# Kernel optimization log

Hardware: AMD Instinct MI355X
Metric: run time of the kernel (lower is better)

The kernel has to match this reference:

```python
import jax, jax.numpy as jnp
import numpy as np

C_S = 128
C_T = 128
C_OUT = 128


def _proj(x, W, b):
    # 1x1x1 Conv3d == per-voxel linear over channel dim. x: [B, Cin, T, H, W]
    return jnp.einsum('oc,bcthw->bothw', W, x) + b[None, :, None, None, None]


def setup_inputs() -> dict:
    key = jax.random.key(0)
    ks = jax.random.split(key, 12)
    B, T, H, W = 4, 4, 32, 32
    spatial_features = jax.random.normal(ks[0], (B, T, C_S, H, W), dtype=jnp.float32)
    temporal_features = jax.random.normal(ks[1], (B, C_T, T, H, W), dtype=jnp.float32)
    def w(k, o, i):
        return jax.random.normal(k, (o, i), dtype=jnp.float32) * (i ** -0.5)
    return {
        'spatial_features': spatial_features,
        'temporal_features': temporal_features,
        'Wq': w(ks[2], C_OUT, C_S), 'bq': jnp.zeros((C_OUT,), jnp.float32),
        'Wk': w(ks[3], C_OUT, C_T), 'bk': jnp.zeros((C_OUT,), jnp.float32),
        'Wv': w(ks[4], C_OUT, C_T), 'bv': jnp.zeros((C_OUT,), jnp.float32),
        'Wo': w(ks[5], C_OUT, C_OUT), 'bo': jnp.zeros((C_OUT,), jnp.float32),
    }


def reference(spatial_features, temporal_features, Wq, bq, Wk, bk, Wv, bv, Wo, bo):
    B, T, C_s, H, W = spatial_features.shape
    N = T * H * W
    scale = C_OUT ** -0.5
    # permute(0,2,1,3,4): [B, T, C_s, H, W] -> [B, C_s, T, H, W]
    x_s = jnp.transpose(spatial_features, (0, 2, 1, 3, 4))
    q = _proj(x_s, Wq, bq)                 # [B, C_out, T, H, W]
    k = _proj(temporal_features, Wk, bk)   # [B, C_out, T, H, W]
    v = _proj(temporal_features, Wv, bv)   # [B, C_out, T, H, W]
    Q = q.reshape(B, C_OUT, N).transpose(0, 2, 1)  # [B, N, C]
    K = k.reshape(B, C_OUT, N)                     # [B, C, N]
    V = v.reshape(B, C_OUT, N).transpose(0, 2, 1)  # [B, N, C]
    attn = jax.nn.softmax(jnp.einsum('bnc,bcm->bnm', Q, K) * scale, axis=2)  # [B, N, N]
    out = jnp.einsum('bnm,bmc->bnc', attn, V)      # [B, N, C]
    out = out.transpose(0, 2, 1).reshape(B, C_OUT, T, H, W)
    return _proj(out, Wo, bo)
```

## Files before the change

kernel.cpp:

```cpp
#include <hip/hip_runtime.h>
#include <cstddef>

#define NDIM 4096
#define SCALE_L2E 0.12751741843533886f
#define BIAS_L2E  11.541560327111707f

typedef _Float16 h8 __attribute__((ext_vector_type(8)));
typedef _Float16 h4 __attribute__((ext_vector_type(4)));
typedef _Float16 h2 __attribute__((ext_vector_type(2)));
typedef float    f4 __attribute__((ext_vector_type(4)));

__device__ __forceinline__ void gld_lds16(const void* g, void* l) {
    __builtin_amdgcn_global_load_lds(
        (const __attribute__((address_space(1))) void*)g,
        (__attribute__((address_space(3))) void*)l, 16, 0, 0);
}

__device__ __forceinline__ h8 cvt_w_frag(const float* wp) {
    const float4 u0 = *(const float4*)wp;
    const float4 u1 = *(const float4*)(wp + 4);
    h8 f;
    f[0]=(_Float16)u0.x; f[1]=(_Float16)u0.y; f[2]=(_Float16)u0.z; f[3]=(_Float16)u0.w;
    f[4]=(_Float16)u1.x; f[5]=(_Float16)u1.y; f[6]=(_Float16)u1.z; f[7]=(_Float16)u1.w;
    return f;
}

__global__ __launch_bounds__(256) void prep_w_kernel(
    const float* __restrict__ Wq, const float* __restrict__ Wk,
    const float* __restrict__ Wv, const float* __restrict__ Wo,
    _Float16* __restrict__ Whf)
{
    const int gid = blockIdx.x * 256 + threadIdx.x;
    const int mat = gid >> 11, rem = gid & 2047;
    const int ot = rem >> 8, ks = (rem >> 6) & 3, l = rem & 63;
    const float* src = mat == 0 ? Wq : mat == 1 ? Wk : mat == 2 ? Wv : Wo;
    const h8 f = cvt_w_frag(src + (size_t)(16 * ot + (l & 15)) * 128 + 32 * ks + 8 * (l >> 4));
    *(h8*)(Whf + (size_t)gid * 8) = f;
}

__global__ __launch_bounds__(256, 3) void proj_qkv_kernel(
    const float* __restrict__ spatial, const float* __restrict__ temporal,
    const _Float16* __restrict__ Whf,
    const float* __restrict__ bq, const float* __restrict__ bk,
    const float* __restrict__ bv,
    _Float16* __restrict__ Qh, _Float16* __restrict__ Kh, _Float16* __restrict__ Vt)
{
    __shared__ __align__(16) _Float16 Xl[32 * 136];
    const int tid = threadIdx.x;
    const int n0  = blockIdx.x * 32;
    const int b   = blockIdx.y;
    const int p   = blockIdx.z;
    const float* __restrict__ bias = (p == 0) ? bq : (p == 1) ? bk : bv;

    {
        const float* src; size_t rs;
        if (p == 0) { const int t = n0 >> 10, hw0 = n0 & 1023;
            src = spatial + (((size_t)(b * 4 + t) * 128) << 10) + hw0; rs = 1024; }
        else { src = temporal + ((size_t)(b * 128) << 12) + n0; rs = 4096; }
        #pragma unroll
        for (int i = 0; i < 2; ++i) {
            const int ii = tid + 256 * i;
            const int c2 = ii >> 3, j = ii & 7;
            const float4 v0 = *(const float4*)(src + (size_t)(2 * c2) * rs + 4 * j);
            const float4 v1 = *(const float4*)(src + (size_t)(2 * c2 + 1) * rs + 4 * j);
            const float a0[4] = {v0.x, v0.y, v0.z, v0.w};
            const float a1[4] = {v1.x, v1.y, v1.z, v1.w};
            #pragma unroll
            for (int u = 0; u < 4; ++u) {
                h2 pk; pk[0] = (_Float16)a0[u]; pk[1] = (_Float16)a1[u];
                *(h2*)&Xl[(4 * j + u) * 136 + 2 * c2] = pk;
            }
        }
    }
    __syncthreads();

    const int w = tid >> 6, lane = tid & 63, n16 = tid & 15, q4 = (tid >> 4) & 3;

    h8 wf[2][4];
    #pragma unroll
    for (int otl = 0; otl < 2; ++otl)
        #pragma unroll
        for (int ks = 0; ks < 4; ++ks)
            wf[otl][ks] = *(const h8*)(Whf + ((size_t)(((p * 8 + 2 * w + otl) * 4 + ks)) << 9)
                                           + lane * 8);
    h8 xf[2][4];
    #pragma unroll
    for (int ns = 0; ns < 2; ++ns)
        #pragma unroll
        for (int ks = 0; ks < 4; ++ks)
            xf[ns][ks] = *(const h8*)&Xl[(16 * ns + n16) * 136 + 32 * ks + 8 * q4];

    if (p < 2) {
        f4 acc[2][2];
        #pragma unroll
        for (int i = 0; i < 2; ++i) { acc[i][0] = (f4)0.0f; acc[i][1] = (f4)0.0f; }
        #pragma unroll
        for (int otl = 0; otl < 2; ++otl)
            #pragma unroll
            for (int ns = 0; ns < 2; ++ns)
                #pragma unroll
                for (int ks = 0; ks < 4; ++ks)
                    acc[otl][ns] = __builtin_amdgcn_mfma_f32_16x16x32_f16(
                        wf[otl][ks], xf[ns][ks], acc[otl][ns], 0, 0, 0);
        _Float16* __restrict__ dst = (p == 0) ? Qh : Kh;
        #pragma unroll
        for (int otl = 0; otl < 2; ++otl) {
            const float4 bb = *(const float4*)&bias[16 * (2 * w + otl) + 4 * q4];
            #pragma unroll
            for (int ns = 0; ns < 2; ++ns) {
                h4 r;
                r[0]=(_Float16)(acc[otl][ns][0]+bb.x); r[1]=(_Float16)(acc[otl][ns][1]+bb.y);
                r[2]=(_Float16)(acc[otl][ns][2]+bb.z); r[3]=(_Float16)(acc[otl][ns][3]+bb.w);
                *(h4*)(dst + ((size_t)b * NDIM + n0 + 16 * ns + n16) * 128
                           + 16 * (2 * w + otl) + 4 * q4) = r;
            }
        }
    } else {
        f4 acc[2][2];
        #pragma unroll
        for (int i = 0; i < 2; ++i) { acc[i][0] = (f4)0.0f; acc[i][1] = (f4)0.0f; }
        #pragma unroll
        for (int ns = 0; ns < 2; ++ns)
            #pragma unroll
            for (int otl = 0; otl < 2; ++otl)
                #pragma unroll
                for (int ks = 0; ks < 4; ++ks)
                    acc[ns][otl] = __builtin_amdgcn_mfma_f32_16x16x32_f16(
                        xf[ns][ks], wf[otl][ks], acc[ns][otl], 0, 0, 0);
        #pragma unroll
        for (int ns = 0; ns < 2; ++ns)
            #pragma unroll
            for (int otl = 0; otl < 2; ++otl) {
                const float bb = bias[16 * (2 * w + otl) + n16];
                h4 r;
                r[0]=(_Float16)(acc[ns][otl][0]+bb); r[1]=(_Float16)(acc[ns][otl][1]+bb);
                r[2]=(_Float16)(acc[ns][otl][2]+bb); r[3]=(_Float16)(acc[ns][otl][3]+bb);
                *(h4*)(Vt + ((size_t)(b * 128 + 16 * (2 * w + otl) + n16) << 12)
                          + n0 + 16 * ns + 4 * q4) = r;
            }
    }
}

__global__ __launch_bounds__(512, 4) void attn_kernel(
    const _Float16* __restrict__ Qh, const _Float16* __restrict__ Kh,
    const _Float16* __restrict__ Vt, _Float16* __restrict__ Opart,
    float* __restrict__ lpart)
{
    __shared__ __align__(16) _Float16 sh[30720];

    const int tid  = threadIdx.x;
    const int w    = tid >> 6, lane = tid & 63;
    const int n16  = lane & 15, q4 = lane >> 4;

    const int id = blockIdx.x + 32 * blockIdx.y + 128 * blockIdx.z;
    const int pi = (id & 7) + 8 * (id >> 8);
    const int qt = (id >> 3) & 31;
    const int hf = pi & 3, b = pi >> 2;
    const int n0 = qt * 128;
    const int mb = hf * 1024;

    const int kr = tid >> 4, kc = tid & 15;
    const _Float16* kg = Kh + ((size_t)b * NDIM + mb + kr) * 128
                            + 8 * (kc ^ (kr & 7));
    const int vr = tid >> 2, vc = tid & 3;
    const _Float16* vg = Vt + (((size_t)(b * 128 + vr)) << 12) + mb
                            + 8 * (vc ^ ((vr >> 1) & 3));
    const int ld = tid * 8;

    gld_lds16(kg, sh + ld);
    gld_lds16(vg, sh + 8192 + ld);
    kg += 32 * 128; vg += 32;

    const int rw = w & 3;
    const int g  = rw >> 1, p = rw & 1;

    if (w < 4) {
        h8 qf[4][4];
        {
            const _Float16* Qb = Qh + ((size_t)b * NDIM + n0 + 64 * g + n16) * 128;
            #pragma unroll
            for (int qs = 0; qs < 4; ++qs)
                #pragma unroll
                for (int ks = 0; ks < 4; ++ks)
                    qf[qs][ks] = *(const h8*)(Qb + (size_t)(16 * qs) * 128 + 32 * ks + 8 * q4);
        }
        float lsum[4] = {0.0f, 0.0f, 0.0f, 0.0f};
        const int kx   = (n16 & 7) << 3;
        const int krow = (16 * p + n16) * 128;
        int vnxt = 1;

        for (int it = 0; it < 32; ++it) {
            __syncthreads();
            const int cur = it & 1;
            if (it < 31) {
                gld_lds16(kg, sh + (cur ^ 1) * 4096 + ld);
                gld_lds16(vg, sh + 8192 + vnxt * 4096 + ld);
                kg += 32 * 128; vg += 32;
                vnxt = vnxt == 2 ? 0 : vnxt + 1;
            }
            f4 sacc[4];
            #pragma unroll
            for (int qs = 0; qs < 4; ++qs) sacc[qs] = (f4)0.0f;
            {
                const _Float16* __restrict__ KB = sh + cur * 4096;
                h8 kf[4];
                #pragma unroll
                for (int ks = 0; ks < 4; ++ks)
                    kf[ks] = *(const h8*)&KB[krow + ((32 * ks + 8 * q4) ^ kx)];
                __builtin_amdgcn_s_setprio(1);
                #pragma unroll
                for (int ks = 0; ks < 4; ++ks)
                    #pragma unroll
                    for (int qs = 0; qs < 4; ++qs)
                        sacc[qs] = __builtin_amdgcn_mfma_f32_16x16x32_f16(
                            kf[ks], qf[qs][ks], sacc[qs], 0, 0, 0);
                __builtin_amdgcn_s_setprio(0);
            }
            _Float16* __restrict__ Pb = sh + 20480 + cur * 5120;
            #pragma unroll
            for (int qs = 0; qs < 4; ++qs) {
                h4 pk;
                #pragma unroll
                for (int r = 0; r < 4; ++r) {
                    const float e = __builtin_amdgcn_exp2f(
                        fmaf(sacc[qs][r], SCALE_L2E, -BIAS_L2E));
                    lsum[qs] += e;
                    pk[r] = (_Float16)e;
                }
                *(h4*)&Pb[(64 * g + 16 * qs + n16) * 40 + 16 * p + 4 * q4] = pk;
            }
        }
        __syncthreads();
        #pragma unroll
        for (int qs = 0; qs < 4; ++qs) {
            lsum[qs] += __shfl_xor(lsum[qs], 16, 64);
            lsum[qs] += __shfl_xor(lsum[qs], 32, 64);
        }
        if (q4 == 0) {
            float* lb = lpart + ((size_t)((hf * 2 + p) * 4 + b)) * NDIM + n0 + 64 * g;
            #pragma unroll
            for (int qs = 0; qs < 4; ++qs) lb[16 * qs + n16] = lsum[qs];
        }
        __syncthreads();
        __syncthreads();
    } else {
        f4 oacc[4][4];
        #pragma unroll
        for (int i = 0; i < 4; ++i)
            #pragma unroll
            for (int j = 0; j < 4; ++j) oacc[i][j] = (f4)0.0f;
        int vnxt = 1, vprv = 0;

        for (int it = 0; it < 32; ++it) {
            __syncthreads();
            const int cur = it & 1;
            if (it < 31) {
                gld_lds16(kg, sh + (cur ^ 1) * 4096 + ld);
                gld_lds16(vg, sh + 8192 + vnxt * 4096 + ld);
                kg += 32 * 128; vg += 32;
                vnxt = vnxt == 2 ? 0 : vnxt + 1;
            }
            if (it > 0) {
                const _Float16* __restrict__ Pp = sh + 20480 + (cur ^ 1) * 5120;
                const _Float16* __restrict__ VP = sh + 8192 + vprv * 4096;
                h8 vf[4];
                #pragma unroll
                for (int ct = 0; ct < 4; ++ct) {
                    const int r = 64 * p + 16 * ct + n16;
                    vf[ct] = *(const h8*)&VP[r * 32 + 8 * (q4 ^ ((r >> 1) & 3))];
                }
                __builtin_amdgcn_s_setprio(1);
                #pragma unroll
                for (int qs = 0; qs < 4; ++qs) {
                    const h8 pf = *(const h8*)&Pp[(64 * g + 16 * qs + n16) * 40 + 8 * q4];
                    #pragma unroll
                    for (int ct = 0; ct < 4; ++ct)
                        oacc[qs][ct] = __builtin_amdgcn_mfma_f32_16x16x32_f16(
                            pf, vf[ct], oacc[qs][ct], 0, 0, 0);
                }
                __builtin_amdgcn_s_setprio(0);
                vprv = vprv == 2 ? 0 : vprv + 1;
            }
        }
        __syncthreads();
        {
            const _Float16* __restrict__ Pp = sh + 20480 + 5120;
            const _Float16* __restrict__ VP = sh + 8192 + 4096;
            h8 vf[4];
            #pragma unroll
            for (int ct = 0; ct < 4; ++ct) {
                const int r = 64 * p + 16 * ct + n16;
                vf[ct] = *(const h8*)&VP[r * 32 + 8 * (q4 ^ ((r >> 1) & 3))];
            }
            #pragma unroll
            for (int qs = 0; qs < 4; ++qs) {
                const h8 pf = *(const h8*)&Pp[(64 * g + 16 * qs + n16) * 40 + 8 * q4];
                #pragma unroll
                for (int ct = 0; ct < 4; ++ct)
                    oacc[qs][ct] = __builtin_amdgcn_mfma_f32_16x16x32_f16(
                        pf, vf[ct], oacc[qs][ct], 0, 0, 0);
            }
        }
        __syncthreads();
        #pragma unroll
        for (int qs = 0; qs < 4; ++qs)
            #pragma unroll
            for (int ct = 0; ct < 4; ++ct)
                #pragma unroll
                for (int r = 0; r < 4; ++r)
                    sh[(64 * g + 16 * qs + 4 * q4 + r) * 136 + 64 * p + 16 * ct + n16] =
                        (_Float16)oacc[qs][ct][r];
        __syncthreads();
    }

    const size_t ob = ((size_t)(hf * 4 + b) * NDIM + n0) * 128;
    #pragma unroll
    for (int i = 0; i < 4; ++i) {
        const int ii  = tid + 512 * i;
        const int row = ii >> 4, c8 = (ii & 15) * 8;
        *(int4*)(Opart + ob + (size_t)row * 128 + c8) = *(const int4*)&sh[row * 136 + c8];
    }
}

__global__ __launch_bounds__(256, 2) void proj_final_kernel(
    const _Float16* __restrict__ Opart, const float* __restrict__ lpart,
    const _Float16* __restrict__ Whf, const float* __restrict__ bo,
    float* __restrict__ out)
{
    __shared__ __align__(16) _Float16 Xl[32 * 136];
    __shared__ float lrow[32];
    __shared__ __align__(16) float Ofin[128 * 36];
    const int tid = threadIdx.x;
    const int n0  = blockIdx.x * 32;
    const int b   = blockIdx.y;

    if (tid < 32) {
        float l = 0.0f;
        #pragma unroll
        for (int h8i = 0; h8i < 8; ++h8i)
            l += lpart[((size_t)(h8i * 4 + b)) * NDIM + n0 + tid];
        lrow[tid] = 1.0f / l;
    }
    float vals[2][8];
    int rows[2], c8s[2];
    #pragma unroll
    for (int i = 0; i < 2; ++i) {
        const int ii = tid + 256 * i;
        rows[i] = ii >> 4; c8s[i] = (ii & 15) * 8;
        #pragma unroll
        for (int j = 0; j < 8; ++j) vals[i][j] = 0.0f;
        #pragma unroll
        for (int hf = 0; hf < 4; ++hf) {
            const h8 o = *(const h8*)(Opart + ((size_t)(hf * 4 + b) * NDIM + n0 + rows[i]) * 128
                                      + c8s[i]);
            #pragma unroll
            for (int j = 0; j < 8; ++j) vals[i][j] += (float)o[j];
        }
    }
    __syncthreads();
    #pragma unroll
    for (int i = 0; i < 2; ++i) {
        const float linv = lrow[rows[i]];
        h8 r;
        #pragma unroll
        for (int j = 0; j < 8; ++j) r[j] = (_Float16)(vals[i][j] * linv);
        *(h8*)&Xl[rows[i] * 136 + c8s[i]] = r;
    }
    __syncthreads();

    const int w = tid >> 6, lane = tid & 63, n16 = tid & 15, q4 = (tid >> 4) & 3;

    h8 wf[2][4];
    #pragma unroll
    for (int otl = 0; otl < 2; ++otl)
        #pragma unroll
        for (int ks = 0; ks < 4; ++ks)
            wf[otl][ks] = *(const h8*)(Whf + ((size_t)(((3 * 8 + 2 * w + otl) * 4 + ks)) << 9)
                                           + lane * 8);
    h8 xf[2][4];
    #pragma unroll
    for (int ns = 0; ns < 2; ++ns)
        #pragma unroll
        for (int ks = 0; ks < 4; ++ks)
            xf[ns][ks] = *(const h8*)&Xl[(16 * ns + n16) * 136 + 32 * ks + 8 * q4];

    f4 acc[2][2];
    #pragma unroll
    for (int i = 0; i < 2; ++i) { acc[i][0] = (f4)0.0f; acc[i][1] = (f4)0.0f; }
    #pragma unroll
    for (int otl = 0; otl < 2; ++otl)
        #pragma unroll
        for (int ns = 0; ns < 2; ++ns)
            #pragma unroll
            for (int ks = 0; ks < 4; ++ks)
                acc[otl][ns] = __builtin_amdgcn_mfma_f32_16x16x32_f16(
                    wf[otl][ks], xf[ns][ks], acc[otl][ns], 0, 0, 0);

    #pragma unroll
    for (int otl = 0; otl < 2; ++otl) {
        const float4 bb = *(const float4*)&bo[16 * (2 * w + otl) + 4 * q4];
        const float bias[4] = {bb.x, bb.y, bb.z, bb.w};
        #pragma unroll
        for (int ns = 0; ns < 2; ++ns)
            #pragma unroll
            for (int r = 0; r < 4; ++r)
                Ofin[(16 * (2 * w + otl) + 4 * q4 + r) * 36 + 16 * ns + n16] =
                    acc[otl][ns][r] + bias[r];
    }
    __syncthreads();
    #pragma unroll
    for (int i = 0; i < 4; ++i) {
        const int ii  = tid + 256 * i;
        const int row = ii >> 3, j = ii & 7;
        *(float4*)(out + (((size_t)(b * 128 + row)) << 12) + n0 + 4 * j) =
            *(const float4*)&Ofin[row * 36 + 4 * j];
    }
}

extern "C" void kernel_launch(void* const* d_in, const int* in_sizes, int n_in,
                              void* d_out, int out_size, void* d_ws, size_t ws_size,
                              hipStream_t stream)
{
    const float* spatial  = (const float*)d_in[0];
    const float* temporal = (const float*)d_in[1];
    const float* Wq = (const float*)d_in[2];
    const float* bq = (const float*)d_in[3];
    const float* Wk = (const float*)d_in[4];
    const float* bk = (const float*)d_in[5];
    const float* Wv = (const float*)d_in[6];
    const float* bv = (const float*)d_in[7];
    const float* Wo = (const float*)d_in[8];
    const float* bo = (const float*)d_in[9];

    char* ws = (char*)d_ws;
    _Float16* Qh    = (_Float16*)(ws);
    _Float16* Kh    = (_Float16*)(ws + (4u  << 20));
    _Float16* Vt    = (_Float16*)(ws + (8u  << 20));
    _Float16* Opart = (_Float16*)(ws + (12u << 20));
    float*    lpart = (float*)   (ws + (28u << 20));
    _Float16* Whf   = (_Float16*)(ws + (28u << 20) + (512u << 10));

    prep_w_kernel<<<32, 256, 0, stream>>>(Wq, Wk, Wv, Wo, Whf);
    proj_qkv_kernel<<<dim3(128, 4, 3), 256, 0, stream>>>(
        spatial, temporal, Whf, bq, bk, bv, Qh, Kh, Vt);
    attn_kernel<<<dim3(32, 4, 4), 512, 0, stream>>>(Qh, Kh, Vt, Opart, lpart);
    proj_final_kernel<<<dim3(128, 4), 256, 0, stream>>>(Opart, lpart, Whf, bo,
                                                        (float*)d_out);
}
```

Before: 134.1 us.

## Deepen K/V LDS prefetch pipeline to two stages ahead with explicit vmcnt waits

The attention kernel's K tile moves from double to triple buffering and its V tile from triple to quadruple buffering in LDS. Two tiles are now prefetched before the loop. Each iteration waits with an explicit s_waitcnt vmcnt(2) followed by a raw s_barrier instead of __syncthreads, so one load group can stay in flight across the barrier. This is meant to hide more global-load latency, at the cost of more LDS per block (about 76KB), which may reduce occupancy, and of fragile hand-written wait counts.

```diff
diff --git a/kernel.cpp b/kernel.cpp
--- a/kernel.cpp
+++ b/kernel.cpp
@@ -146,7 +146,7 @@
     const _Float16* __restrict__ Vt, _Float16* __restrict__ Opart,
     float* __restrict__ lpart)
 {
-    __shared__ __align__(16) _Float16 sh[30720];
+    __shared__ __align__(16) _Float16 sh[38912];
 
     const int tid  = threadIdx.x;
     const int w    = tid >> 6, lane = tid & 63;
@@ -168,7 +168,10 @@
     const int ld = tid * 8;
 
     gld_lds16(kg, sh + ld);
-    gld_lds16(vg, sh + 8192 + ld);
+    gld_lds16(vg, sh + 12288 + ld);
+    kg += 32 * 128; vg += 32;
+    gld_lds16(kg, sh + 4096 + ld);
+    gld_lds16(vg, sh + 16384 + ld);
     kg += 32 * 128; vg += 32;
 
     const int rw = w & 3;
@@ -187,22 +190,30 @@
         float lsum[4] = {0.0f, 0.0f, 0.0f, 0.0f};
         const int kx   = (n16 & 7) << 3;
         const int krow = (16 * p + n16) * 128;
-        int vnxt = 1;
+        int kst = 2, vst = 2;
+        int kcu = 0;
 
         for (int it = 0; it < 32; ++it) {
-            __syncthreads();
-            const int cur = it & 1;
             if (it < 31) {
-                gld_lds16(kg, sh + (cur ^ 1) * 4096 + ld);
-                gld_lds16(vg, sh + 8192 + vnxt * 4096 + ld);
+                asm volatile("s_waitcnt vmcnt(2) lgkmcnt(0)" ::: "memory");
+            } else {
+                asm volatile("s_waitcnt vmcnt(0) lgkmcnt(0)" ::: "memory");
+            }
+            __builtin_amdgcn_s_barrier();
+            __builtin_amdgcn_sched_barrier(0);
+            if (it < 30) {
+                gld_lds16(kg, sh + kst * 4096 + ld);
+                gld_lds16(vg, sh + 12288 + vst * 4096 + ld);
                 kg += 32 * 128; vg += 32;
-                vnxt = vnxt == 2 ? 0 : vnxt + 1;
-            }
+                kst = kst == 2 ? 0 : kst + 1;
+                vst = (vst + 1) & 3;
+            }
+
             f4 sacc[4];
             #pragma unroll
             for (int qs = 0; qs < 4; ++qs) sacc[qs] = (f4)0.0f;
             {
-                const _Float16* __restrict__ KB = sh + cur * 4096;
+                const _Float16* __restrict__ KB = sh + kcu * 4096;
                 h8 kf[4];
                 #pragma unroll
                 for (int ks = 0; ks < 4; ++ks)
@@ -216,7 +227,9 @@
                             kf[ks], qf[qs][ks], sacc[qs], 0, 0, 0);
                 __builtin_amdgcn_s_setprio(0);
             }
-            _Float16* __restrict__ Pb = sh + 20480 + cur * 5120;
+            kcu = kcu == 2 ? 0 : kcu + 1;
+
+            _Float16* __restrict__ Pb = sh + 28672 + (it & 1) * 5120;
             #pragma unroll
             for (int qs = 0; qs < 4; ++qs) {
                 h4 pk;
@@ -249,20 +262,27 @@
         for (int i = 0; i < 4; ++i)
             #pragma unroll
             for (int j = 0; j < 4; ++j) oacc[i][j] = (f4)0.0f;
-        int vnxt = 1, vprv = 0;
+        int kst = 2, vst = 2;
 
         for (int it = 0; it < 32; ++it) {
-            __syncthreads();
-            const int cur = it & 1;
             if (it < 31) {
-                gld_lds16(kg, sh + (cur ^ 1) * 4096 + ld);
-                gld_lds16(vg, sh + 8192 + vnxt * 4096 + ld);
+                asm volatile("s_waitcnt vmcnt(2) lgkmcnt(0)" ::: "memory");
+            } else {
+                asm volatile("s_waitcnt vmcnt(0) lgkmcnt(0)" ::: "memory");
+            }
+            __builtin_amdgcn_s_barrier();
+            __builtin_amdgcn_sched_barrier(0);
+            if (it < 30) {
+                gld_lds16(kg, sh + kst * 4096 + ld);
+                gld_lds16(vg, sh + 12288 + vst * 4096 + ld);
                 kg += 32 * 128; vg += 32;
-                vnxt = vnxt == 2 ? 0 : vnxt + 1;
-            }
+                kst = kst == 2 ? 0 : kst + 1;
+                vst = (vst + 1) & 3;
+            }
+
             if (it > 0) {
-                const _Float16* __restrict__ Pp = sh + 20480 + (cur ^ 1) * 5120;
-                const _Float16* __restrict__ VP = sh + 8192 + vprv * 4096;
+                const _Float16* __restrict__ Pp = sh + 28672 + ((it & 1) ^ 1) * 5120;
+                const _Float16* __restrict__ VP = sh + 12288 + ((it - 1) & 3) * 4096;
                 h8 vf[4];
                 #pragma unroll
                 for (int ct = 0; ct < 4; ++ct) {
@@ -279,13 +299,12 @@
                             pf, vf[ct], oacc[qs][ct], 0, 0, 0);
                 }
                 __builtin_amdgcn_s_setprio(0);
-                vprv = vprv == 2 ? 0 : vprv + 1;
             }
         }
         __syncthreads();
         {
-            const _Float16* __restrict__ Pp = sh + 20480 + 5120;
-            const _Float16* __restrict__ VP = sh + 8192 + 4096;
+            const _Float16* __restrict__ Pp = sh + 28672 + 5120;
+            const _Float16* __restrict__ VP = sh + 12288 + 3 * 4096;
             h8 vf[4];
             #pragma unroll
             for (int ct = 0; ct < 4; ++ct) {
```

Result: no change. 132.6 us, median of 2 (-1.1%).
